# Kernel optimization log

Measured on AMD Instinct MI355X. Metric: run time of the kernel, lower is better.

The kernel has to match this reference:

```python
import jax, jax.numpy as jnp
import numpy as np

EPS = 1e-8  # torch F.cosine_similarity eps


def _f_m(v1, v2, Wl):
    """Weighted multi-perspective cosine sim. v1,v2: [s,B,D], Wl: [l,D] -> [s,B,l]."""
    a = v1[:, :, None, :] * Wl  # [s,B,l,D]
    b = v2[:, :, None, :] * Wl
    num = jnp.sum(a * b, axis=-1)
    den = jnp.linalg.norm(a, axis=-1) * jnp.linalg.norm(b, axis=-1)
    return num / jnp.maximum(den, EPS)


def _maxpool_match(p, q, Wl):
    """f_m_multi followed by max over q positions. p,q: [s,B,D], Wl: [l,D] -> [s,B,l]."""
    pw = p[:, :, None, :] * Wl  # [s,B,l,D]
    qw = q[:, :, None, :] * Wl  # [t,B,l,D]
    num = jnp.einsum('sbld,tbld->stbl', pw, qw)
    n1 = jnp.linalg.norm(pw, axis=-1)  # [s,B,l]
    n2 = jnp.linalg.norm(qw, axis=-1)  # [t,B,l]
    sim = num / jnp.maximum(n1[:, None] * n2[None], EPS)  # [s,t,B,l]
    return sim.max(axis=1)


def _attentive_match(p, q, W0, W1):
    """p,q: [s,B,D]; W0,W1: [l,D] -> (m_att, m_maxatt) each [s,B,l]."""
    num = jnp.einsum('sbd,tbd->stb', p, q)
    np_ = jnp.linalg.norm(p, axis=-1)  # [s,B]
    nq_ = jnp.linalg.norm(q, axis=-1)  # [t,B]
    alpha = num / jnp.maximum(np_[:, None] * nq_[None], EPS)  # [s,t,B]
    h_mean = jnp.einsum('stb,tbd->sbd', alpha, q) / alpha.sum(axis=1)[:, :, None]
    m_att = _f_m(p, h_mean, W0)
    idx = jnp.argmax(alpha, axis=1)  # [s,B] index into q seq dim
    B = q.shape[1]
    h_maxatt = q[idx, jnp.arange(B)[None, :], :]  # [s,B,D]
    m_maxatt = _f_m(p, h_maxatt, W1)
    return m_att, m_maxatt


def setup_inputs() -> dict:
    key = jax.random.key(0)
    k1, k2, k3 = jax.random.split(key, 3)
    s, B, D2, l = 256, 128, 512, 8
    p_contexts = jax.random.normal(k1, (s, B, D2), dtype=jnp.float32)
    q_contexts = jax.random.normal(k2, (s, B, D2), dtype=jnp.float32)
    W = jax.random.normal(k3, (8, l, D2 // 2), dtype=jnp.float32)
    return {"p_contexts": p_contexts, "q_contexts": q_contexts, "W": W}


def reference(p_contexts, q_contexts, W):
    half = p_contexts.shape[-1] // 2
    p_fw, p_bw = p_contexts[..., :half], p_contexts[..., half:]
    q_fw, q_bw = q_contexts[..., :half], q_contexts[..., half:]
    shp = p_fw.shape
    # full matching: p vs last fw / first bw q state
    m_full_fw = _f_m(p_fw, jnp.broadcast_to(q_fw[-1], shp), W[0])
    m_full_bw = _f_m(p_bw, jnp.broadcast_to(q_bw[0], shp), W[1])
    # maxpool matching
    m_max_fw = _maxpool_match(p_fw, q_fw, W[2])
    m_max_bw = _maxpool_match(p_bw, q_bw, W[3])
    # attentive + max-attentive matching (original uses W[4], W[5] for both directions)
    m_att_fw, m_maxatt_fw = _attentive_match(p_fw, q_fw, W[4], W[5])
    m_att_bw, m_maxatt_bw = _attentive_match(p_bw, q_bw, W[4], W[5])
    return jnp.concatenate(
        [m_full_fw, m_full_bw, m_max_fw, m_max_bw,
         m_att_fw, m_att_bw, m_maxatt_fw, m_maxatt_bw], axis=-1)
```

## Files before the change

kernel.cpp:

```cpp
#include <hip/hip_runtime.h>
#include <hip/hip_bf16.h>

#define EPSF 1e-8f

typedef __attribute__((ext_vector_type(8))) __bf16 bf16x8;
typedef __attribute__((ext_vector_type(4))) float f32x4;

constexpr int S = 256;
constexpr int NB = 128;
constexpr int D2 = 512;
constexpr int HALF = 256;
constexpr int NBD2 = NB * D2;
constexpr size_t NORM_ELEMS = (size_t)2 * 33 * NB * S;

constexpr size_t OFF_ASUM  = 17301504;
constexpr size_t OFF_AIDX  = 17563648;
constexpr size_t OFF_QHI   = 17825792;
constexpr size_t OFF_QLO   = 51380224;
constexpr size_t OFF_QT    = 84934656;
constexpr size_t OFF_ALPHA = 118489088;
constexpr size_t WS_NEED   = 152043520;

__device__ __forceinline__ size_t normIdx(int dir, int slot, int b, int row) {
    return (((size_t)dir * 33 + slot) * NB + b) * S + row;
}

__device__ __forceinline__ uint pack2bf(float a, float b) {
    __hip_bfloat162 t = __float22bfloat162_rn(make_float2(a, b));
    uint u;
    __builtin_memcpy(&u, &t, 4);
    return u;
}

__device__ __forceinline__ bf16x8 ld8(const __bf16* p8) {
    union { uint2 u[2]; bf16x8 v; } t;
    t.u[0] = *(const uint2*)p8;
    t.u[1] = *(const uint2*)(p8 + 4);
    return t.v;
}

__global__ __launch_bounds__(256) void k_norms(const float* __restrict__ p,
                                               const float* __restrict__ q,
                                               const float* __restrict__ W,
                                               float* __restrict__ ws)
{
    int blk = blockIdx.x;
    int b = blk & 127;
    int dir = (blk >> 7) & 1;
    int tensor = blk >> 8;
    const float* x = tensor ? q : p;
    float* outN = ws + (size_t)tensor * NORM_ELEMS;

    __shared__ float W2[32][HALF];
    for (int e = threadIdx.x; e < 32 * HALF; e += 256) {
        int slot = e >> 8;
        int d = e & (HALF - 1);
        int wl = slot >> 3, l = slot & 7;
        int wi = (wl == 0) ? dir : (wl == 1) ? (2 + dir) : (wl == 2) ? 4 : 5;
        float w = W[(size_t)(wi * 8 + l) * HALF + d];
        W2[slot][d] = w * w;
    }
    __syncthreads();

    int row = threadIdx.x;
    const float* xr = x + ((size_t)row * NB + b) * D2 + dir * HALF;
    float acc[33];
#pragma unroll
    for (int i = 0; i < 33; i++) acc[i] = 0.f;
    for (int d4 = 0; d4 < HALF; d4 += 4) {
        float4 v = *(const float4*)(xr + d4);
        float xx = v.x * v.x, yy = v.y * v.y, zz = v.z * v.z, ww = v.w * v.w;
        acc[32] += xx + yy + zz + ww;
#pragma unroll
        for (int slot = 0; slot < 32; slot++) {
            acc[slot] += xx * W2[slot][d4] + yy * W2[slot][d4 + 1]
                       + zz * W2[slot][d4 + 2] + ww * W2[slot][d4 + 3];
        }
    }
#pragma unroll
    for (int slot = 0; slot < 33; slot++)
        outN[normIdx(dir, slot, b, row)] = sqrtf(acc[slot]);
}

__global__ __launch_bounds__(256) void k_packA(const float* __restrict__ q,
                                               char* __restrict__ wsb)
{
    int blk = blockIdx.x;
    int tt = blk & 3;
    int b = (blk >> 2) & 127;
    int dir = blk >> 9;
    int tid = threadIdx.x;
    int t = tt * 64 + (tid >> 2);
    int dpart = (tid & 3) * 64;
    const float* src = q + ((size_t)t * NB + b) * D2 + dir * HALF + dpart;
    size_t so = (((size_t)(dir * 128 + b)) << 16) + (size_t)t * 256 + dpart;
    __bf16* qhi = (__bf16*)(wsb + OFF_QHI) + so;
    __bf16* qlo = (__bf16*)(wsb + OFF_QLO) + so;
#pragma unroll
    for (int j = 0; j < 64; j += 8) {
        float4 v0 = *(const float4*)(src + j);
        float4 v1 = *(const float4*)(src + j + 4);
        uint h0 = pack2bf(v0.x, v0.y), h1 = pack2bf(v0.z, v0.w);
        uint h2 = pack2bf(v1.x, v1.y), h3 = pack2bf(v1.z, v1.w);
        *(uint4*)(qhi + j) = make_uint4(h0, h1, h2, h3);
        uint l0 = pack2bf(v0.x - __uint_as_float(h0 << 16),
                          v0.y - __uint_as_float(h0 & 0xffff0000u));
        uint l1 = pack2bf(v0.z - __uint_as_float(h1 << 16),
                          v0.w - __uint_as_float(h1 & 0xffff0000u));
        uint l2 = pack2bf(v1.x - __uint_as_float(h2 << 16),
                          v1.y - __uint_as_float(h2 & 0xffff0000u));
        uint l3 = pack2bf(v1.z - __uint_as_float(h3 << 16),
                          v1.w - __uint_as_float(h3 & 0xffff0000u));
        *(uint4*)(qlo + j) = make_uint4(l0, l1, l2, l3);
    }
}

__global__ __launch_bounds__(256) void k_packT(char* __restrict__ wsb)
{
    int blk = blockIdx.x;
    const __bf16* qhi = (const __bf16*)(wsb + OFF_QHI) + ((size_t)blk << 16);
    __bf16* qt = (__bf16*)(wsb + OFF_QT) + ((size_t)blk << 16);
    __shared__ __align__(16) __bf16 tile[64 * 264];
    int tid = threadIdx.x;
    for (int dt = 0; dt < 4; dt++) {
        {
            const __bf16* srow = qhi + (size_t)tid * 256 + dt * 64;
#pragma unroll
            for (int j0 = 0; j0 < 64; j0 += 8) {
                union { uint4 u; __bf16 h[8]; } v;
                v.u = *(const uint4*)(srow + j0);
#pragma unroll
                for (int j = 0; j < 8; j++) tile[(j0 + j) * 264 + tid] = v.h[j];
            }
        }
        __syncthreads();
        {
            int d = tid >> 2, tq = tid & 3;
            const uint4* srcl = (const uint4*)&tile[d * 264 + tq * 64];
            uint4* dst = (uint4*)(qt + (size_t)(dt * 64 + d) * 256 + tq * 64);
#pragma unroll
            for (int j = 0; j < 8; j++) dst[j] = srcl[j];
        }
        __syncthreads();
    }
}

__global__ __launch_bounds__(256) void k_full(const float* __restrict__ p,
                                              const float* __restrict__ q,
                                              const float* __restrict__ W,
                                              const float* __restrict__ ws,
                                              float* __restrict__ out)
{
    int blk = blockIdx.x;
    int bg = blk & 3;
    int s = (blk >> 2) & 255;
    int dir = blk >> 10;
    int tid = threadIdx.x;
    int b = bg * 32 + (tid >> 3);
    int l = tid & 7;
    int wi = dir;

    __shared__ float W2[8][HALF];
    for (int e = tid; e < 8 * HALF; e += 256) {
        int ll = e >> 8, d = e & (HALF - 1);
        float w = W[(size_t)(wi * 8 + ll) * HALF + d];
        W2[ll][d] = w * w;
    }
    __syncthreads();

    int qrow = dir ? 0 : (S - 1);
    const float* pr = p + ((size_t)s * NB + b) * D2 + dir * HALF;
    const float* qr = q + ((size_t)qrow * NB + b) * D2 + dir * HALF;
    float num = 0.f;
    for (int d4 = 0; d4 < HALF; d4 += 4) {
        float4 pv = *(const float4*)(pr + d4);
        float4 qv = *(const float4*)(qr + d4);
        num += pv.x * qv.x * W2[l][d4] + pv.y * qv.y * W2[l][d4 + 1]
             + pv.z * qv.z * W2[l][d4 + 2] + pv.w * qv.w * W2[l][d4 + 3];
    }
    const float* normP = ws;
    const float* normQ = ws + NORM_ELEMS;
    float n1 = normP[normIdx(dir, l, b, s)];
    float n2 = normQ[normIdx(dir, l, b, qrow)];
    out[((size_t)s * NB + b) * 64 + dir * 8 + l] = num / fmaxf(n1 * n2, EPSF);
}

__global__ __launch_bounds__(256) void k_maxpool3(const float* __restrict__ p,
                                                  const float* __restrict__ W,
                                                  const char* __restrict__ wsb,
                                                  float* __restrict__ out)
{
    int grp = blockIdx.x & 255;
    int sub = blockIdx.x >> 8;
    int b = grp & 127, dir = grp >> 7;
    int lp = sub >> 2, sc = sub & 3;
    int l0 = lp * 2;
    int s0 = sc * 64;
    int wi = 2 + dir;
    int tid = threadIdx.x;

    __shared__ __align__(16) __bf16 Al[2][64][40];
    __shared__ __align__(16) __bf16 Bl[256][40];
    __shared__ __align__(16) float W2L[2][HALF];
    __shared__ float n1l[2][64];
    __shared__ float n2l[2][HALF];
    __shared__ float wmax[2][4][64];

    const float* normP = (const float*)wsb;
    const float* normQ = normP + NORM_ELEMS;
    const __bf16* qh = (const __bf16*)(wsb + OFF_QHI) + ((size_t)(dir * 128 + b) << 16);

    {
        int e = tid;
#pragma unroll
        for (int ll = 0; ll < 2; ll++) {
            float w = W[(size_t)(wi * 8 + l0 + ll) * HALF + e];
            W2L[ll][e] = w * w;
            n2l[ll][e] = normQ[normIdx(dir, 8 + l0 + ll, b, e)];
        }
    }
    if (tid < 64) {
#pragma unroll
        for (int ll = 0; ll < 2; ll++)
            n1l[ll][tid] = normP[normIdx(dir, 8 + l0 + ll, b, s0 + tid)];
    }

    int wave = tid >> 6, lane = tid & 63;
    int colq = lane & 15, quad = lane >> 4;

    f32x4 acc[2][4][4];
#pragma unroll
    for (int ll = 0; ll < 2; ll++)
#pragma unroll
        for (int mi = 0; mi < 4; mi++)
#pragma unroll
            for (int ni = 0; ni < 4; ni++)
#pragma unroll
                for (int k = 0; k < 4; k++) acc[ll][mi][ni][k] = 0.f;

    const float* pbase = p + (size_t)b * D2 + dir * HALF;

    for (int k0 = 0; k0 < HALF; k0 += 32) {
        __syncthreads();
        {
            const uint4* src = (const uint4*)(qh + (size_t)tid * 256 + k0);
            uint4* dst = (uint4*)&Bl[tid][0];
            dst[0] = src[0]; dst[1] = src[1]; dst[2] = src[2]; dst[3] = src[3];
        }
        {
            int row = tid >> 2, cg = (tid & 3) * 8;
            const float* pr = pbase + (size_t)(s0 + row) * NBD2 + k0 + cg;
            float4 v0 = *(const float4*)pr;
            float4 v1 = *(const float4*)(pr + 4);
#pragma unroll
            for (int ll = 0; ll < 2; ll++) {
                float4 w0 = *(const float4*)&W2L[ll][k0 + cg];
                float4 w1 = *(const float4*)&W2L[ll][k0 + cg + 4];
                uint u0 = pack2bf(v0.x * w0.x, v0.y * w0.y);
                uint u1 = pack2bf(v0.z * w0.z, v0.w * w0.w);
                uint u2 = pack2bf(v1.x * w1.x, v1.y * w1.y);
                uint u3 = pack2bf(v1.z * w1.z, v1.w * w1.w);
                *(uint4*)&Al[ll][row][cg] = make_uint4(u0, u1, u2, u3);
            }
        }
        __syncthreads();
        {
            int kk = quad * 8;
            bf16x8 bfr[4];
#pragma unroll
            for (int ni = 0; ni < 4; ni++)
                bfr[ni] = *(const bf16x8*)&Bl[wave * 64 + ni * 16 + colq][kk];
#pragma unroll
            for (int ll = 0; ll < 2; ll++) {
                bf16x8 afl[4];
#pragma unroll
                for (int mi = 0; mi < 4; mi++)
                    afl[mi] = *(const bf16x8*)&Al[ll][mi * 16 + colq][kk];
#pragma unroll
                for (int mi = 0; mi < 4; mi++)
#pragma unroll
                    for (int ni = 0; ni < 4; ni++)
                        acc[ll][mi][ni] = __builtin_amdgcn_mfma_f32_16x16x32_bf16(
                            afl[mi], bfr[ni], acc[ll][mi][ni], 0, 0, 0);
            }
        }
    }

#pragma unroll
    for (int ll = 0; ll < 2; ll++) {
#pragma unroll
        for (int mi = 0; mi < 4; mi++) {
#pragma unroll
            for (int rg = 0; rg < 4; rg++) {
                int sl = mi * 16 + quad * 4 + rg;
                float n1v = n1l[ll][sl];
                float m = -3.4e38f;
#pragma unroll
                for (int ni = 0; ni < 4; ni++) {
                    int t = wave * 64 + ni * 16 + colq;
                    float sim = acc[ll][mi][ni][rg] / fmaxf(n1v * n2l[ll][t], EPSF);
                    m = fmaxf(m, sim);
                }
#pragma unroll
                for (int msk = 1; msk < 16; msk <<= 1)
                    m = fmaxf(m, __shfl_xor(m, msk, 64));
                if (colq == 0) wmax[ll][wave][sl] = m;
            }
        }
    }
    __syncthreads();
    if (tid < 128) {
        int ll = tid >> 6, sl = tid & 63;
        float m = fmaxf(fmaxf(wmax[ll][0][sl], wmax[ll][1][sl]),
                        fmaxf(wmax[ll][2][sl], wmax[ll][3][sl]));
        out[((size_t)(s0 + sl) * NB + b) * 64 + 16 + dir * 8 + l0 + ll] = m;
    }
}

__global__ __launch_bounds__(256) void k_alpha(const float* __restrict__ p,
                                               char* __restrict__ wsb)
{
    int blk = blockIdx.x;
    int grp = blk & 255;
    int st = blk >> 8;
    int b = grp & 127, dir = grp >> 7;
    int s0 = st * 64;
    int tid = threadIdx.x;
    int wave = tid >> 6, lane = tid & 63;
    int colq = lane & 15, quad = lane >> 4;

    const float* normP = (const float*)wsb;
    const float* normQ = normP + NORM_ELEMS;
    size_t slice = (size_t)(dir * 128 + b) << 16;
    const __bf16* qh = (const __bf16*)(wsb + OFF_QHI) + slice;
    const __bf16* ql = (const __bf16*)(wsb + OFF_QLO) + slice;
    __bf16* aW = (__bf16*)(wsb + OFF_ALPHA) + slice;
    float* asumW = (float*)(wsb + OFF_ASUM) + (size_t)(dir * 128 + b) * 256;
    int* aidxW = (int*)(wsb + OFF_AIDX) + (size_t)(dir * 128 + b) * 256;

    __shared__ __align__(16) __bf16 QhiL[256][36];
    __shared__ __align__(16) __bf16 QloL[256][36];
    __shared__ __align__(16) __bf16 PhiL[64][36];
    __shared__ __align__(16) __bf16 PloL[64][36];
    __shared__ float redS[4][64];
    __shared__ float redM[4][64];
    __shared__ int   redI[4][64];

    const float* pbase = p + (size_t)b * D2 + dir * HALF;

    f32x4 acc[4][4];
#pragma unroll
    for (int mi = 0; mi < 4; mi++)
#pragma unroll
        for (int ni = 0; ni < 4; ni++)
#pragma unroll
            for (int k = 0; k < 4; k++) acc[mi][ni][k] = 0.f;

    for (int k0 = 0; k0 < HALF; k0 += 32) {
        __syncthreads();
        {
            const uint4* sh = (const uint4*)(qh + (size_t)tid * 256 + k0);
            const uint4* sl_ = (const uint4*)(ql + (size_t)tid * 256 + k0);
            uint2* dh = (uint2*)&QhiL[tid][0];
            uint2* dl = (uint2*)&QloL[tid][0];
#pragma unroll
            for (int j = 0; j < 4; j++) {
                uint4 v = sh[j];
                dh[2 * j] = make_uint2(v.x, v.y);
                dh[2 * j + 1] = make_uint2(v.z, v.w);
                uint4 w = sl_[j];
                dl[2 * j] = make_uint2(w.x, w.y);
                dl[2 * j + 1] = make_uint2(w.z, w.w);
            }
        }
        {
            int row = tid >> 2, cg = (tid & 3) * 8;
            const float* pr = pbase + (size_t)(s0 + row) * NBD2 + k0 + cg;
            float4 v0 = *(const float4*)pr;
            float4 v1 = *(const float4*)(pr + 4);
            uint h0 = pack2bf(v0.x, v0.y), h1 = pack2bf(v0.z, v0.w);
            uint h2 = pack2bf(v1.x, v1.y), h3 = pack2bf(v1.z, v1.w);
            uint l0 = pack2bf(v0.x - __uint_as_float(h0 << 16),
                              v0.y - __uint_as_float(h0 & 0xffff0000u));
            uint l1 = pack2bf(v0.z - __uint_as_float(h1 << 16),
                              v0.w - __uint_as_float(h1 & 0xffff0000u));
            uint l2 = pack2bf(v1.x - __uint_as_float(h2 << 16),
                              v1.y - __uint_as_float(h2 & 0xffff0000u));
            uint l3 = pack2bf(v1.z - __uint_as_float(h3 << 16),
                              v1.w - __uint_as_float(h3 & 0xffff0000u));
            uint2* dh = (uint2*)&PhiL[row][cg];
            uint2* dl = (uint2*)&PloL[row][cg];
            dh[0] = make_uint2(h0, h1); dh[1] = make_uint2(h2, h3);
            dl[0] = make_uint2(l0, l1); dl[1] = make_uint2(l2, l3);
        }
        __syncthreads();
        {
            int kk = quad * 8;
            bf16x8 ah[4], al_[4], bh[4], bl_[4];
#pragma unroll
            for (int mi = 0; mi < 4; mi++) {
                ah[mi] = ld8(&PhiL[mi * 16 + colq][kk]);
                al_[mi] = ld8(&PloL[mi * 16 + colq][kk]);
            }
#pragma unroll
            for (int ni = 0; ni < 4; ni++) {
                bh[ni] = ld8(&QhiL[wave * 64 + ni * 16 + colq][kk]);
                bl_[ni] = ld8(&QloL[wave * 64 + ni * 16 + colq][kk]);
            }
#pragma unroll
            for (int mi = 0; mi < 4; mi++)
#pragma unroll
                for (int ni = 0; ni < 4; ni++) {
                    acc[mi][ni] = __builtin_amdgcn_mfma_f32_16x16x32_bf16(
                        ah[mi], bh[ni], acc[mi][ni], 0, 0, 0);
                    acc[mi][ni] = __builtin_amdgcn_mfma_f32_16x16x32_bf16(
                        ah[mi], bl_[ni], acc[mi][ni], 0, 0, 0);
                    acc[mi][ni] = __builtin_amdgcn_mfma_f32_16x16x32_bf16(
                        al_[mi], bh[ni], acc[mi][ni], 0, 0, 0);
                }
        }
    }

    float nqv[4];
#pragma unroll
    for (int ni = 0; ni < 4; ni++)
        nqv[ni] = normQ[normIdx(dir, 32, b, wave * 64 + ni * 16 + colq)];

#pragma unroll
    for (int mi = 0; mi < 4; mi++) {
        int rowbase = mi * 16 + quad * 4;
        float npa[4];
#pragma unroll
        for (int rg = 0; rg < 4; rg++)
            npa[rg] = normP[normIdx(dir, 32, b, s0 + rowbase + rg)];
        float av[4][4];
#pragma unroll
        for (int ni = 0; ni < 4; ni++)
#pragma unroll
            for (int rg = 0; rg < 4; rg++)
                av[ni][rg] = acc[mi][ni][rg] / fmaxf(npa[rg] * nqv[ni], EPSF);
#pragma unroll
        for (int ni = 0; ni < 4; ni++)
#pragma unroll
            for (int rg = 0; rg < 4; rg++)
                aW[(size_t)(s0 + rowbase + rg) * 256 + wave * 64 + ni * 16 + colq] =
                    (__bf16)av[ni][rg];
#pragma unroll
        for (int rg = 0; rg < 4; rg++) {
            float sm = av[0][rg] + av[1][rg] + av[2][rg] + av[3][rg];
            float mx = av[0][rg];
            int ix = wave * 64 + colq;
#pragma unroll
            for (int ni = 1; ni < 4; ni++) {
                if (av[ni][rg] > mx) { mx = av[ni][rg]; ix = wave * 64 + ni * 16 + colq; }
            }
#pragma unroll
            for (int off = 1; off < 16; off <<= 1) {
                sm += __shfl_xor(sm, off, 64);
                float m2 = __shfl_xor(mx, off, 64);
                int i2 = __shfl_xor(ix, off, 64);
                if (m2 > mx || (m2 == mx && i2 < ix)) { mx = m2; ix = i2; }
            }
            if (colq == 0) {
                redS[wave][rowbase + rg] = sm;
                redM[wave][rowbase + rg] = mx;
                redI[wave][rowbase + rg] = ix;
            }
        }
    }
    __syncthreads();
    if (tid < 64) {
        float sm = redS[0][tid] + redS[1][tid] + redS[2][tid] + redS[3][tid];
        float mx = redM[0][tid];
        int ix = redI[0][tid];
#pragma unroll
        for (int w = 1; w < 4; w++) {
            float m2 = redM[w][tid];
            int i2 = redI[w][tid];
            if (m2 > mx || (m2 == mx && i2 < ix)) { mx = m2; ix = i2; }
        }
        asumW[s0 + tid] = sm;
        aidxW[s0 + tid] = ix;
    }
}

__global__ __launch_bounds__(256) void k_hout(const float* __restrict__ p,
                                              const float* __restrict__ W,
                                              char* __restrict__ wsb,
                                              float* __restrict__ out)
{
    int blk = blockIdx.x;
    int grp = blk & 255;
    int st = blk >> 8;
    int b = grp & 127, dir = grp >> 7;
    int s0 = st * 64;
    int tid = threadIdx.x;
    int wave = tid >> 6, lane = tid & 63;
    int colq = lane & 15, quad = lane >> 4;

    const float* normP = (const float*)wsb;
    const float* normQ = normP + NORM_ELEMS;
    size_t slice = (size_t)(dir * 128 + b) << 16;
    const __bf16* qh = (const __bf16*)(wsb + OFF_QHI) + slice;
    const __bf16* qt = (const __bf16*)(wsb + OFF_QT) + slice;
    const __bf16* aW = (const __bf16*)(wsb + OFF_ALPHA) + slice;
    const float* asumW = (const float*)(wsb + OFF_ASUM) + (size_t)(dir * 128 + b) * 256;
    const int* aidxW = (const int*)(wsb + OFF_AIDX) + (size_t)(dir * 128 + b) * 256;

    __shared__ __align__(16) char reg0[46080];
    __bf16* alphaA = (__bf16*)reg0;
    __bf16* QTl = alphaA + 64 * 72;
    __bf16* E = (__bf16*)reg0;
    __bf16* W45 = E + 64 * 264;
    __shared__ int   aidxL[64];
    __shared__ float asumL[64];

    if (tid < 64) { aidxL[tid] = aidxW[s0 + tid]; asumL[tid] = asumW[s0 + tid]; }

    const float* pbase = p + (size_t)b * D2 + dir * HALF;

    f32x4 acc[4][4];
#pragma unroll
    for (int mi = 0; mi < 4; mi++)
#pragma unroll
        for (int ni = 0; ni < 4; ni++)
#pragma unroll
            for (int k = 0; k < 4; k++) acc[mi][ni][k] = 0.f;

    for (int tc = 0; tc < 4; tc++) {
        __syncthreads();
        {
            int row = tid >> 2, cp = (tid & 3) * 16;
            const uint4* src = (const uint4*)(aW + (size_t)(s0 + row) * 256 + tc * 64 + cp);
            uint4* dst = (uint4*)&alphaA[row * 72 + cp];
            dst[0] = src[0]; dst[1] = src[1];
        }
        {
            const uint4* src = (const uint4*)(qt + (size_t)tid * 256 + tc * 64);
            uint4* dst = (uint4*)&QTl[tid * 72];
#pragma unroll
            for (int j = 0; j < 8; j++) dst[j] = src[j];
        }
        __syncthreads();
#pragma unroll
        for (int step = 0; step < 2; step++) {
            int kk = step * 32 + quad * 8;
            bf16x8 af[4], bfr[4];
#pragma unroll
            for (int mi = 0; mi < 4; mi++)
                af[mi] = *(const bf16x8*)&alphaA[(mi * 16 + colq) * 72 + kk];
#pragma unroll
            for (int ni = 0; ni < 4; ni++)
                bfr[ni] = *(const bf16x8*)&QTl[(wave * 64 + ni * 16 + colq) * 72 + kk];
#pragma unroll
            for (int mi = 0; mi < 4; mi++)
#pragma unroll
                for (int ni = 0; ni < 4; ni++)
                    acc[mi][ni] = __builtin_amdgcn_mfma_f32_16x16x32_bf16(
                        af[mi], bfr[ni], acc[mi][ni], 0, 0, 0);
        }
    }

    __syncthreads();
    {
        int n = tid >> 4, dblk = (tid & 15) * 16;
        int wrow = (n < 8) ? (4 * 8 + n) : (5 * 8 + (n - 8));
        const float* wr = W + (size_t)wrow * HALF + dblk;
        float4 a = *(const float4*)wr;
        float4 bq = *(const float4*)(wr + 4);
        float4 c = *(const float4*)(wr + 8);
        float4 d4 = *(const float4*)(wr + 12);
        uint u0 = pack2bf(a.x * a.x, a.y * a.y), u1 = pack2bf(a.z * a.z, a.w * a.w);
        uint u2 = pack2bf(bq.x * bq.x, bq.y * bq.y), u3 = pack2bf(bq.z * bq.z, bq.w * bq.w);
        uint u4 = pack2bf(c.x * c.x, c.y * c.y), u5 = pack2bf(c.z * c.z, c.w * c.w);
        uint u6 = pack2bf(d4.x * d4.x, d4.y * d4.y), u7 = pack2bf(d4.z * d4.z, d4.w * d4.w);
        uint4* dst = (uint4*)&W45[n * 264 + dblk];
        dst[0] = make_uint4(u0, u1, u2, u3);
        dst[1] = make_uint4(u4, u5, u6, u7);
    }

    f32x4 c1, c2, c3;
#pragma unroll
    for (int k = 0; k < 4; k++) { c1[k] = 0.f; c2[k] = 0.f; c3[k] = 0.f; }

#pragma unroll
    for (int mi = 0; mi < 4; mi++)
#pragma unroll
        for (int rg = 0; rg < 4; rg++) {
            int sl = mi * 16 + quad * 4 + rg;
            const float* prow = pbase + (size_t)(s0 + sl) * NBD2;
#pragma unroll
            for (int ni = 0; ni < 4; ni++) {
                int d = wave * 64 + ni * 16 + colq;
                E[sl * 264 + d] = (__bf16)(prow[d] * acc[mi][ni][rg]);
            }
        }
    __syncthreads();
#pragma unroll
    for (int step = 0; step < 8; step++) {
        int kk = step * 32 + quad * 8;
        bf16x8 ea = *(const bf16x8*)&E[(wave * 16 + colq) * 264 + kk];
        bf16x8 wb = *(const bf16x8*)&W45[colq * 264 + kk];
        c1 = __builtin_amdgcn_mfma_f32_16x16x32_bf16(ea, wb, c1, 0, 0, 0);
    }
    __syncthreads();

#pragma unroll
    for (int mi = 0; mi < 4; mi++)
#pragma unroll
        for (int rg = 0; rg < 4; rg++) {
            int sl = mi * 16 + quad * 4 + rg;
#pragma unroll
            for (int ni = 0; ni < 4; ni++) {
                int d = wave * 64 + ni * 16 + colq;
                float hv = acc[mi][ni][rg];
                E[sl * 264 + d] = (__bf16)(hv * hv);
            }
        }
    __syncthreads();
#pragma unroll
    for (int step = 0; step < 8; step++) {
        int kk = step * 32 + quad * 8;
        bf16x8 ea = *(const bf16x8*)&E[(wave * 16 + colq) * 264 + kk];
        bf16x8 wb = *(const bf16x8*)&W45[colq * 264 + kk];
        c2 = __builtin_amdgcn_mfma_f32_16x16x32_bf16(ea, wb, c2, 0, 0, 0);
    }
    __syncthreads();

#pragma unroll
    for (int mi = 0; mi < 4; mi++)
#pragma unroll
        for (int rg = 0; rg < 4; rg++) {
            int sl = mi * 16 + quad * 4 + rg;
            const float* prow = pbase + (size_t)(s0 + sl) * NBD2;
            const __bf16* qrow = qh + (size_t)aidxL[sl] * 256;
#pragma unroll
            for (int ni = 0; ni < 4; ni++) {
                int d = wave * 64 + ni * 16 + colq;
                E[sl * 264 + d] = (__bf16)(prow[d] * (float)qrow[d]);
            }
        }
    __syncthreads();
#pragma unroll
    for (int step = 0; step < 8; step++) {
        int kk = step * 32 + quad * 8;
        bf16x8 ea = *(const bf16x8*)&E[(wave * 16 + colq) * 264 + kk];
        bf16x8 wb = *(const bf16x8*)&W45[colq * 264 + kk];
        c3 = __builtin_amdgcn_mfma_f32_16x16x32_bf16(ea, wb, c3, 0, 0, 0);
    }

#pragma unroll
    for (int rg = 0; rg < 4; rg++) {
        int sl = wave * 16 + quad * 4 + rg;
        size_t ob = ((size_t)(s0 + sl) * NB + b) * 64;
        if (colq < 8) {
            int l = colq;
            float np4 = normP[normIdx(dir, 16 + l, b, s0 + sl)];
            float nh = sqrtf(fmaxf(c2[rg], 0.f));
            float sgn = (asumL[sl] < 0.f) ? -1.f : 1.f;
            out[ob + 32 + dir * 8 + l] = sgn * c1[rg] / fmaxf(np4 * nh, EPSF);
        } else {
            int l = colq - 8;
            float np5 = normP[normIdx(dir, 24 + l, b, s0 + sl)];
            float nq5 = normQ[normIdx(dir, 24 + l, b, aidxL[sl])];
            out[ob + 48 + dir * 8 + l] = c3[rg] / fmaxf(np5 * nq5, EPSF);
        }
    }
}

extern "C" void kernel_launch(void* const* d_in, const int* in_sizes, int n_in,
                              void* d_out, int out_size, void* d_ws, size_t ws_size,
                              hipStream_t stream)
{
    (void)in_sizes; (void)n_in; (void)out_size;
    if (ws_size < WS_NEED) return;
    const float* p = (const float*)d_in[0];
    const float* q = (const float*)d_in[1];
    const float* W = (const float*)d_in[2];
    float* out = (float*)d_out;
    float* ws = (float*)d_ws;
    char* wsb = (char*)d_ws;

    hipLaunchKernelGGL(k_norms, dim3(512), dim3(256), 0, stream, p, q, W, ws);
    hipLaunchKernelGGL(k_packA, dim3(1024), dim3(256), 0, stream, q, wsb);
    hipLaunchKernelGGL(k_packT, dim3(256), dim3(256), 0, stream, wsb);
    hipLaunchKernelGGL(k_full, dim3(2048), dim3(256), 0, stream, p, q, W, ws, out);
    hipLaunchKernelGGL(k_maxpool3, dim3(4096), dim3(256), 0, stream, p, W, wsb, out);
    hipLaunchKernelGGL(k_alpha, dim3(1024), dim3(256), 0, stream, p, wsb);
    hipLaunchKernelGGL(k_hout, dim3(1024), dim3(256), 0, stream, p, W, wsb, out);
}
```

Measured before the change: 870.0 us.

## Register-prefetch next K tile and retune LDS row padding across GEMM kernels

In the maxpool, alpha and hout kernels, the next K-chunk of global data is now loaded into registers right after the barrier and overlaps with the MFMA work on the current chunk. Each chunk is then written to LDS at the start of the next iteration. LDS row strides change from 40/72/264 to 36/68/260 bf16 elements, with 8-byte split stores and loads, to reduce bank conflicts and LDS footprint. The cost is higher register pressure from the prefetch buffers, which could lower occupancy.

```diff
diff --git a/kernel.cpp b/kernel.cpp
--- a/kernel.cpp
+++ b/kernel.cpp
@@ -37,6 +37,11 @@
     t.u[0] = *(const uint2*)p8;
     t.u[1] = *(const uint2*)(p8 + 4);
     return t.v;
+}
+
+__device__ __forceinline__ void st16_u2(__bf16* dst, uint4 v) {
+    *(uint2*)dst = make_uint2(v.x, v.y);
+    *(uint2*)(dst + 4) = make_uint2(v.z, v.w);
 }
 
 __global__ __launch_bounds__(256) void k_norms(const float* __restrict__ p,
@@ -185,7 +190,7 @@
     out[((size_t)s * NB + b) * 64 + dir * 8 + l] = num / fmaxf(n1 * n2, EPSF);
 }
 
-__global__ __launch_bounds__(256) void k_maxpool3(const float* __restrict__ p,
+__global__ __launch_bounds__(256) void k_maxpool4(const float* __restrict__ p,
                                                   const float* __restrict__ W,
                                                   const char* __restrict__ wsb,
                                                   float* __restrict__ out)
@@ -199,8 +204,8 @@
     int wi = 2 + dir;
     int tid = threadIdx.x;
 
-    __shared__ __align__(16) __bf16 Al[2][64][40];
-    __shared__ __align__(16) __bf16 Bl[256][40];
+    __shared__ __align__(16) __bf16 Al[2][64][36];
+    __shared__ __align__(16) __bf16 Bl[256][36];
     __shared__ __align__(16) float W2L[2][HALF];
     __shared__ float n1l[2][64];
     __shared__ float n2l[2][HALF];
@@ -227,6 +232,7 @@
 
     int wave = tid >> 6, lane = tid & 63;
     int colq = lane & 15, quad = lane >> 4;
+    int arow = tid >> 2, acg = (tid & 3) * 8;
 
     f32x4 acc[2][4][4];
 #pragma unroll
@@ -240,42 +246,57 @@
 
     const float* pbase = p + (size_t)b * D2 + dir * HALF;
 
-    for (int k0 = 0; k0 < HALF; k0 += 32) {
+    uint4 breg[4];
+    float4 av0, av1;
+    {
+        const uint4* src = (const uint4*)(qh + (size_t)tid * 256);
+        breg[0] = src[0]; breg[1] = src[1]; breg[2] = src[2]; breg[3] = src[3];
+        const float* pr = pbase + (size_t)(s0 + arow) * NBD2 + acg;
+        av0 = *(const float4*)pr;
+        av1 = *(const float4*)(pr + 4);
+    }
+
+    for (int kc = 0; kc < 8; kc++) {
+        int k0 = kc * 32;
         __syncthreads();
         {
-            const uint4* src = (const uint4*)(qh + (size_t)tid * 256 + k0);
-            uint4* dst = (uint4*)&Bl[tid][0];
-            dst[0] = src[0]; dst[1] = src[1]; dst[2] = src[2]; dst[3] = src[3];
-        }
-        {
-            int row = tid >> 2, cg = (tid & 3) * 8;
-            const float* pr = pbase + (size_t)(s0 + row) * NBD2 + k0 + cg;
-            float4 v0 = *(const float4*)pr;
-            float4 v1 = *(const float4*)(pr + 4);
+            __bf16* dst = &Bl[tid][0];
+            st16_u2(dst, breg[0]); st16_u2(dst + 8, breg[1]);
+            st16_u2(dst + 16, breg[2]); st16_u2(dst + 24, breg[3]);
+        }
+        {
 #pragma unroll
             for (int ll = 0; ll < 2; ll++) {
-                float4 w0 = *(const float4*)&W2L[ll][k0 + cg];
-                float4 w1 = *(const float4*)&W2L[ll][k0 + cg + 4];
-                uint u0 = pack2bf(v0.x * w0.x, v0.y * w0.y);
-                uint u1 = pack2bf(v0.z * w0.z, v0.w * w0.w);
-                uint u2 = pack2bf(v1.x * w1.x, v1.y * w1.y);
-                uint u3 = pack2bf(v1.z * w1.z, v1.w * w1.w);
-                *(uint4*)&Al[ll][row][cg] = make_uint4(u0, u1, u2, u3);
+                float4 w0 = *(const float4*)&W2L[ll][k0 + acg];
+                float4 w1 = *(const float4*)&W2L[ll][k0 + acg + 4];
+                uint u0 = pack2bf(av0.x * w0.x, av0.y * w0.y);
+                uint u1 = pack2bf(av0.z * w0.z, av0.w * w0.w);
+                uint u2 = pack2bf(av1.x * w1.x, av1.y * w1.y);
+                uint u3 = pack2bf(av1.z * w1.z, av1.w * w1.w);
+                st16_u2(&Al[ll][arow][acg], make_uint4(u0, u1, u2, u3));
             }
         }
         __syncthreads();
+        if (kc < 7) {
+            int kn = k0 + 32;
+            const uint4* src = (const uint4*)(qh + (size_t)tid * 256 + kn);
+            breg[0] = src[0]; breg[1] = src[1]; breg[2] = src[2]; breg[3] = src[3];
+            const float* pr = pbase + (size_t)(s0 + arow) * NBD2 + kn + acg;
+            av0 = *(const float4*)pr;
+            av1 = *(const float4*)(pr + 4);
+        }
         {
             int kk = quad * 8;
             bf16x8 bfr[4];
 #pragma unroll
             for (int ni = 0; ni < 4; ni++)
-                bfr[ni] = *(const bf16x8*)&Bl[wave * 64 + ni * 16 + colq][kk];
+                bfr[ni] = ld8(&Bl[wave * 64 + ni * 16 + colq][kk]);
 #pragma unroll
             for (int ll = 0; ll < 2; ll++) {
                 bf16x8 afl[4];
 #pragma unroll
                 for (int mi = 0; mi < 4; mi++)
-                    afl[mi] = *(const bf16x8*)&Al[ll][mi * 16 + colq][kk];
+                    afl[mi] = ld8(&Al[ll][mi * 16 + colq][kk]);
 #pragma unroll
                 for (int mi = 0; mi < 4; mi++)
 #pragma unroll
@@ -347,6 +368,7 @@
     __shared__ int   redI[4][64];
 
     const float* pbase = p + (size_t)b * D2 + dir * HALF;
+    int prow_ = tid >> 2, pcg = (tid & 3) * 8;
 
     f32x4 acc[4][4];
 #pragma unroll
@@ -356,44 +378,61 @@
 #pragma unroll
             for (int k = 0; k < 4; k++) acc[mi][ni][k] = 0.f;
 
-    for (int k0 = 0; k0 < HALF; k0 += 32) {
+    uint4 qhR[2], qlR[2];
+    float4 pv0, pv1;
+    {
+        const uint4* sh = (const uint4*)(qh + (size_t)tid * 256);
+        const uint4* sl_ = (const uint4*)(ql + (size_t)tid * 256);
+        qhR[0] = sh[0]; qhR[1] = sh[1];
+        qlR[0] = sl_[0]; qlR[1] = sl_[1];
+        const float* pr = pbase + (size_t)(s0 + prow_) * NBD2 + pcg;
+        pv0 = *(const float4*)pr;
+        pv1 = *(const float4*)(pr + 4);
+    }
+    uint4 qhR2[2], qlR2[2];
+    {
+        const uint4* sh = (const uint4*)(qh + (size_t)tid * 256);
+        const uint4* sl_ = (const uint4*)(ql + (size_t)tid * 256);
+        qhR2[0] = sh[2]; qhR2[1] = sh[3];
+        qlR2[0] = sl_[2]; qlR2[1] = sl_[3];
+    }
+
+    for (int kc = 0; kc < 8; kc++) {
+        int k0 = kc * 32;
         __syncthreads();
         {
-            const uint4* sh = (const uint4*)(qh + (size_t)tid * 256 + k0);
-            const uint4* sl_ = (const uint4*)(ql + (size_t)tid * 256 + k0);
-            uint2* dh = (uint2*)&QhiL[tid][0];
-            uint2* dl = (uint2*)&QloL[tid][0];
-#pragma unroll
-            for (int j = 0; j < 4; j++) {
-                uint4 v = sh[j];
-                dh[2 * j] = make_uint2(v.x, v.y);
-                dh[2 * j + 1] = make_uint2(v.z, v.w);
-                uint4 w = sl_[j];
-                dl[2 * j] = make_uint2(w.x, w.y);
-                dl[2 * j + 1] = make_uint2(w.z, w.w);
-            }
-        }
-        {
-            int row = tid >> 2, cg = (tid & 3) * 8;
-            const float* pr = pbase + (size_t)(s0 + row) * NBD2 + k0 + cg;
-            float4 v0 = *(const float4*)pr;
-            float4 v1 = *(const float4*)(pr + 4);
-            uint h0 = pack2bf(v0.x, v0.y), h1 = pack2bf(v0.z, v0.w);
-            uint h2 = pack2bf(v1.x, v1.y), h3 = pack2bf(v1.z, v1.w);
-            uint l0 = pack2bf(v0.x - __uint_as_float(h0 << 16),
-                              v0.y - __uint_as_float(h0 & 0xffff0000u));
-            uint l1 = pack2bf(v0.z - __uint_as_float(h1 << 16),
-                              v0.w - __uint_as_float(h1 & 0xffff0000u));
-            uint l2 = pack2bf(v1.x - __uint_as_float(h2 << 16),
-                              v1.y - __uint_as_float(h2 & 0xffff0000u));
-            uint l3 = pack2bf(v1.z - __uint_as_float(h3 << 16),
-                              v1.w - __uint_as_float(h3 & 0xffff0000u));
-            uint2* dh = (uint2*)&PhiL[row][cg];
-            uint2* dl = (uint2*)&PloL[row][cg];
-            dh[0] = make_uint2(h0, h1); dh[1] = make_uint2(h2, h3);
-            dl[0] = make_uint2(l0, l1); dl[1] = make_uint2(l2, l3);
+            __bf16* dh = &QhiL[tid][0];
+            __bf16* dl = &QloL[tid][0];
+            st16_u2(dh, qhR[0]); st16_u2(dh + 8, qhR[1]);
+            st16_u2(dh + 16, qhR2[0]); st16_u2(dh + 24, qhR2[1]);
+            st16_u2(dl, qlR[0]); st16_u2(dl + 8, qlR[1]);
+            st16_u2(dl + 16, qlR2[0]); st16_u2(dl + 24, qlR2[1]);
+        }
+        {
+            uint h0 = pack2bf(pv0.x, pv0.y), h1 = pack2bf(pv0.z, pv0.w);
+            uint h2 = pack2bf(pv1.x, pv1.y), h3 = pack2bf(pv1.z, pv1.w);
+            uint l0 = pack2bf(pv0.x - __uint_as_float(h0 << 16),
+                              pv0.y - __uint_as_float(h0 & 0xffff0000u));
+            uint l1 = pack2bf(pv0.z - __uint_as_float(h1 << 16),
+                              pv0.w - __uint_as_float(h1 & 0xffff0000u));
+            uint l2 = pack2bf(pv1.x - __uint_as_float(h2 << 16),
+                              pv1.y - __uint_as_float(h2 & 0xffff0000u));
+            uint l3 = pack2bf(pv1.z - __uint_as_float(h3 << 16),
+                              pv1.w - __uint_as_float(h3 & 0xffff0000u));
+            st16_u2(&PhiL[prow_][pcg], make_uint4(h0, h1, h2, h3));
+            st16_u2(&PloL[prow_][pcg], make_uint4(l0, l1, l2, l3));
         }
         __syncthreads();
+        if (kc < 7) {
+            int kn = k0 + 32;
+            const uint4* sh = (const uint4*)(qh + (size_t)tid * 256 + kn);
+            const uint4* sl_ = (const uint4*)(ql + (size_t)tid * 256 + kn);
+            qhR[0] = sh[0]; qhR[1] = sh[1]; qhR2[0] = sh[2]; qhR2[1] = sh[3];
+            qlR[0] = sl_[0]; qlR[1] = sl_[1]; qlR2[0] = sl_[2]; qlR2[1] = sl_[3];
+            const float* pr = pbase + (size_t)(s0 + prow_) * NBD2 + kn + pcg;
+            pv0 = *(const float4*)pr;
+            pv1 = *(const float4*)(pr + 4);
+        }
         {
             int kk = quad * 8;
             bf16x8 ah[4], al_[4], bh[4], bl_[4];
@@ -507,11 +546,11 @@
     const float* asumW = (const float*)(wsb + OFF_ASUM) + (size_t)(dir * 128 + b) * 256;
     const int* aidxW = (const int*)(wsb + OFF_AIDX) + (size_t)(dir * 128 + b) * 256;
 
-    __shared__ __align__(16) char reg0[46080];
+    __shared__ __align__(16) char reg0[43520];
     __bf16* alphaA = (__bf16*)reg0;
-    __bf16* QTl = alphaA + 64 * 72;
+    __bf16* QTl = alphaA + 64 * 68;
     __bf16* E = (__bf16*)reg0;
-    __bf16* W45 = E + 64 * 264;
+    __bf16* W45 = E + 64 * 260;
     __shared__ int   aidxL[64];
     __shared__ float asumL[64];
 
@@ -527,31 +566,42 @@
 #pragma unroll
             for (int k = 0; k < 4; k++) acc[mi][ni][k] = 0.f;
 
+    int arow = tid >> 2, acp = (tid & 3) * 16;
+    uint4 aR[2], qR[8];
+    {
+        const uint4* src = (const uint4*)(aW + (size_t)(s0 + arow) * 256 + acp);
+        aR[0] = src[0]; aR[1] = src[1];
+        const uint4* sq = (const uint4*)(qt + (size_t)tid * 256);
+#pragma unroll
+        for (int j = 0; j < 8; j++) qR[j] = sq[j];
+    }
     for (int tc = 0; tc < 4; tc++) {
         __syncthreads();
         {
-            int row = tid >> 2, cp = (tid & 3) * 16;
-            const uint4* src = (const uint4*)(aW + (size_t)(s0 + row) * 256 + tc * 64 + cp);
-            uint4* dst = (uint4*)&alphaA[row * 72 + cp];
-            dst[0] = src[0]; dst[1] = src[1];
-        }
-        {
-            const uint4* src = (const uint4*)(qt + (size_t)tid * 256 + tc * 64);
-            uint4* dst = (uint4*)&QTl[tid * 72];
-#pragma unroll
-            for (int j = 0; j < 8; j++) dst[j] = src[j];
+            __bf16* dst = &alphaA[arow * 68 + acp];
+            st16_u2(dst, aR[0]); st16_u2(dst + 8, aR[1]);
+            __bf16* dq = &QTl[tid * 68];
+#pragma unroll
+            for (int j = 0; j < 8; j++) st16_u2(dq + j * 8, qR[j]);
         }
         __syncthreads();
+        if (tc < 3) {
+            const uint4* src = (const uint4*)(aW + (size_t)(s0 + arow) * 256 + (tc + 1) * 64 + acp);
+            aR[0] = src[0]; aR[1] = src[1];
+            const uint4* sq = (const uint4*)(qt + (size_t)tid * 256 + (tc + 1) * 64);
+#pragma unroll
+            for (int j = 0; j < 8; j++) qR[j] = sq[j];
+        }
 #pragma unroll
         for (int step = 0; step < 2; step++) {
             int kk = step * 32 + quad * 8;
             bf16x8 af[4], bfr[4];
 #pragma unroll
             for (int mi = 0; mi < 4; mi++)
-                af[mi] = *(const bf16x8*)&alphaA[(mi * 16 + colq) * 72 + kk];
+                af[mi] = ld8(&alphaA[(mi * 16 + colq) * 68 + kk]);
 #pragma unroll
             for (int ni = 0; ni < 4; ni++)
-                bfr[ni] = *(const bf16x8*)&QTl[(wave * 64 + ni * 16 + colq) * 72 + kk];
+                bfr[ni] = ld8(&QTl[(wave * 64 + ni * 16 + colq) * 68 + kk]);
 #pragma unroll
             for (int mi = 0; mi < 4; mi++)
 #pragma unroll
@@ -574,9 +624,9 @@
         uint u2 = pack2bf(bq.x * bq.x, bq.y * bq.y), u3 = pack2bf(bq.z * bq.z, bq.w * bq.w);
         uint u4 = pack2bf(c.x * c.x, c.y * c.y), u5 = pack2bf(c.z * c.z, c.w * c.w);
         uint u6 = pack2bf(d4.x * d4.x, d4.y * d4.y), u7 = pack2bf(d4.z * d4.z, d4.w * d4.w);
-        uint4* dst = (uint4*)&W45[n * 264 + dblk];
-        dst[0] = make_uint4(u0, u1, u2, u3);
-        dst[1] = make_uint4(u4, u5, u6, u7);
+        __bf16* dst = &W45[n * 260 + dblk];
+        st16_u2(dst, make_uint4(u0, u1, u2, u3));
+        st16_u2(dst + 8, make_uint4(u4, u5, u6, u7));
     }
 
     f32x4 c1, c2, c3;
@@ -592,15 +642,15 @@
 #pragma unroll
             for (int ni = 0; ni < 4; ni++) {
                 int d = wave * 64 + ni * 16 + colq;
-                E[sl * 264 + d] = (__bf16)(prow[d] * acc[mi][ni][rg]);
+                E[sl * 260 + d] = (__bf16)(prow[d] * acc[mi][ni][rg]);
             }
         }
     __syncthreads();
 #pragma unroll
     for (int step = 0; step < 8; step++) {
         int kk = step * 32 + quad * 8;
-        bf16x8 ea = *(const bf16x8*)&E[(wave * 16 + colq) * 264 + kk];
-        bf16x8 wb = *(const bf16x8*)&W45[colq * 264 + kk];
+        bf16x8 ea = ld8(&E[(wave * 16 + colq) * 260 + kk]);
+        bf16x8 wb = ld8(&W45[colq * 260 + kk]);
         c1 = __builtin_amdgcn_mfma_f32_16x16x32_bf16(ea, wb, c1, 0, 0, 0);
     }
     __syncthreads();
@@ -614,15 +664,15 @@
             for (int ni = 0; ni < 4; ni++) {
                 int d = wave * 64 + ni * 16 + colq;
                 float hv = acc[mi][ni][rg];
-                E[sl * 264 + d] = (__bf16)(hv * hv);
+                E[sl * 260 + d] = (__bf16)(hv * hv);
             }
         }
     __syncthreads();
 #pragma unroll
     for (int step = 0; step < 8; step++) {
         int kk = step * 32 + quad * 8;
-        bf16x8 ea = *(const bf16x8*)&E[(wave * 16 + colq) * 264 + kk];
-        bf16x8 wb = *(const bf16x8*)&W45[colq * 264 + kk];
+        bf16x8 ea = ld8(&E[(wave * 16 + colq) * 260 + kk]);
+        bf16x8 wb = ld8(&W45[colq * 260 + kk]);
         c2 = __builtin_amdgcn_mfma_f32_16x16x32_bf16(ea, wb, c2, 0, 0, 0);
     }
     __syncthreads();
@@ -637,15 +687,15 @@
 #pragma unroll
             for (int ni = 0; ni < 4; ni++) {
                 int d = wave * 64 + ni * 16 + colq;
-                E[sl * 264 + d] = (__bf16)(prow[d] * (float)qrow[d]);
+                E[sl * 260 + d] = (__bf16)(prow[d] * (float)qrow[d]);
             }
         }
     __syncthreads();
 #pragma unroll
     for (int step = 0; step < 8; step++) {
         int kk = step * 32 + quad * 8;
-        bf16x8 ea = *(const bf16x8*)&E[(wave * 16 + colq) * 264 + kk];
-        bf16x8 wb = *(const bf16x8*)&W45[colq * 264 + kk];
+        bf16x8 ea = ld8(&E[(wave * 16 + colq) * 260 + kk]);
+        bf16x8 wb = ld8(&W45[colq * 260 + kk]);
         c3 = __builtin_amdgcn_mfma_f32_16x16x32_bf16(ea, wb, c3, 0, 0, 0);
     }
 
@@ -685,7 +735,7 @@
     hipLaunchKernelGGL(k_packA, dim3(1024), dim3(256), 0, stream, q, wsb);
     hipLaunchKernelGGL(k_packT, dim3(256), dim3(256), 0, stream, wsb);
     hipLaunchKernelGGL(k_full, dim3(2048), dim3(256), 0, stream, p, q, W, ws, out);
-    hipLaunchKernelGGL(k_maxpool3, dim3(4096), dim3(256), 0, stream, p, W, wsb, out);
+    hipLaunchKernelGGL(k_maxpool4, dim3(4096), dim3(256), 0, stream, p, W, wsb, out);
     hipLaunchKernelGGL(k_alpha, dim3(1024), dim3(256), 0, stream, p, wsb);
     hipLaunchKernelGGL(k_hout, dim3(1024), dim3(256), 0, stream, p, W, wsb, out);
 }
```

New measurement: 844.6 us. 2.9% less time.
